# Optimization experiments

Measured on AMD Instinct MI355X. Metric: run time of the kernel, lower is better.

The kernel has to match this reference:

```python
import jax, jax.numpy as jnp
import numpy as np

TOP_K = 2
NUM_EXPERTS = 8
CAPACITY_FACTOR = 1.0


def setup_inputs() -> dict:
    key = jax.random.key(0)
    k1, k2, k3, k4 = jax.random.split(key, 4)
    sl, bs, hs, ffn = 2048, 2, 1024, 4096
    x = jax.random.normal(k1, (sl, bs, hs), dtype=jnp.float32)
    router_w = jax.random.normal(k2, (hs, NUM_EXPERTS), dtype=jnp.float32) * 0.02
    w1 = jax.random.normal(k3, (NUM_EXPERTS, hs, ffn), dtype=jnp.float32) * 0.02
    w2 = jax.random.normal(k4, (NUM_EXPERTS, ffn, hs), dtype=jnp.float32) * 0.02
    bias = jnp.zeros((1, 1, hs), dtype=jnp.float32)
    return {"x": x, "router_w": router_w, "w1": w1, "w2": w2, "bias": bias}


def _moe_forward(x, router_w, w1, w2):
    sl, bs, hs = x.shape
    xf = x.reshape(-1, hs)                                   # [T, H]
    T = xf.shape[0]
    TK = T * TOP_K
    capacity = int(CAPACITY_FACTOR * TOP_K * T / NUM_EXPERTS)  # static

    # Router: softmax over experts, then top-k (LearnedRouter)
    scores = jax.nn.softmax(xf @ router_w, axis=-1)          # [T, E]
    expert_weights, top_experts = jax.lax.top_k(scores, TOP_K)  # [T, K]
    ew = expert_weights.reshape(-1)                          # [T*K]
    te = top_experts.reshape(-1).astype(jnp.int32)           # [T*K]

    # indices_and_bins: stable sort by expert id + histogram + inclusive cumsum
    indices = jnp.argsort(te, stable=True)                   # sorted pos -> flat slot
    tokens_per_expert = jnp.zeros((NUM_EXPERTS,), jnp.int32).at[te].add(1)
    bins = jnp.cumsum(tokens_per_expert)                     # inclusive cumsum
    starts = bins - tokens_per_expert                        # exclusive offsets

    # binned_gather -> [E, capacity, H]; tokens beyond capacity are dropped
    c_range = jnp.arange(capacity)
    pos = starts[:, None] + c_range[None, :]                 # [E, C] positions in sorted order
    valid = c_range[None, :] < tokens_per_expert[:, None]    # [E, C]
    slot = indices[jnp.clip(pos, 0, TK - 1)]                 # flat (token*K + k) slot
    tok = slot // TOP_K                                      # source token row
    gathered = jnp.where(valid[..., None], xf[tok], 0.0)     # [E, C, H]

    # grouped expert MLP: gelu(x @ w1) @ w2  (megablocks mlp.MLP)
    h = jax.nn.gelu(jnp.einsum('ech,ehf->ecf', gathered, w1))
    y = jnp.einsum('ecf,efh->ech', h, w2)                    # [E, C, H]

    # binned_scatter: weighted accumulate back to token rows
    p = jnp.arange(TK)
    e_of_p = jnp.searchsorted(bins, p, side='right')         # expert of sorted pos
    c_of_p = p - starts[e_of_p]                              # slot within expert bin
    ok = c_of_p < capacity                                   # dropped tokens contribute 0
    vals = jnp.where(ok[:, None], y[e_of_p, jnp.clip(c_of_p, 0, capacity - 1)], 0.0)
    flat = indices                                           # flat slot at sorted pos p
    w = ew[flat]
    out = jnp.zeros((T, hs), x.dtype).at[flat // TOP_K].add(w[:, None] * vals)
    return out.reshape(sl, bs, hs)


def reference(x, router_w, w1, w2, bias):
    out = _moe_forward(x, router_w, w1, w2)
    return (out, bias)
```

## Files before the change

kernel.cpp:

```cpp
#include <hip/hip_runtime.h>
#include <hip/hip_bf16.h>


#define T_TOK 4096
#define HS 1024
#define FFN 4096
#define NE 8
#define CAP 1024
#define TKS 8192

#define WS_TE   67108864
#define WS_EW   67141632
#define WS_PERM 67174400
#define WS_WT   67239936
#define WS_XB   134348800

typedef float f4 __attribute__((ext_vector_type(4)));
typedef __bf16 bf16x8 __attribute__((ext_vector_type(8)));
typedef float f32x4 __attribute__((ext_vector_type(4)));

__device__ __forceinline__ void gld_lds16(const void* g, void* l) {
    __builtin_amdgcn_global_load_lds(
        (const __attribute__((address_space(1))) unsigned int*)g,
        (__attribute__((address_space(3))) unsigned int*)l, 16, 0, 0);
}

__global__ void init_out_kernel(float* __restrict__ out, const float* __restrict__ bias) {
    int i = blockIdx.x * 256 + threadIdx.x;
    const int TH = T_TOK * HS;
    if (i < TH) out[i] = 0.0f;
    else if (i < TH + HS) out[i] = bias[i - TH];
}

__global__ __launch_bounds__(256) void router_kernel(const float* __restrict__ x,
                                                     const float* __restrict__ rw,
                                                     int* __restrict__ te,
                                                     float* __restrict__ ew,
                                                     __bf16* __restrict__ xb) {
    __shared__ float rwt[NE * HS];
    int tid = threadIdx.x;
    for (int i = tid; i < NE * HS; i += 256) {
        int h = i >> 3, e = i & 7;
        rwt[e * HS + h] = rw[i];
    }
    __syncthreads();
    int wave = tid >> 6, lane = tid & 63;
    int t = blockIdx.x * 4 + wave;
    const float* xr = x + (size_t)t * HS;
    float s[NE];
    float xv[16];
#pragma unroll
    for (int e = 0; e < NE; ++e) s[e] = 0.0f;
#pragma unroll
    for (int j = 0; j < 16; ++j) {
        int h = lane + j * 64;
        xv[j] = xr[h];
#pragma unroll
        for (int e = 0; e < NE; ++e) s[e] += xv[j] * rwt[e * HS + h];
    }
#pragma unroll
    for (int j = 0; j < 16; ++j)
        xb[(size_t)t * HS + lane + j * 64] = (__bf16)xv[j];
#pragma unroll
    for (int e = 0; e < NE; ++e) {
#pragma unroll
        for (int off = 1; off < 64; off <<= 1) s[e] += __shfl_xor(s[e], off, 64);
    }
    float m = s[0];
#pragma unroll
    for (int e = 1; e < NE; ++e) m = fmaxf(m, s[e]);
    float psum = 0.0f;
#pragma unroll
    for (int e = 0; e < NE; ++e) psum += __expf(s[e] - m);
    int e0 = 0; float v0 = s[0];
#pragma unroll
    for (int e = 1; e < NE; ++e) { if (s[e] > v0) { v0 = s[e]; e0 = e; } }
    int e1 = -1; float v1 = -1e30f;
#pragma unroll
    for (int e = 0; e < NE; ++e) { if (e != e0 && s[e] > v1) { v1 = s[e]; e1 = e; } }
    if (lane == 0) {
        float inv = 1.0f / psum;
        te[2 * t]     = e0;
        te[2 * t + 1] = e1;
        ew[2 * t]     = __expf(v0 - m) * inv;
        ew[2 * t + 1] = __expf(v1 - m) * inv;
    }
}

__global__ __launch_bounds__(256) void sort_kernel(const int* __restrict__ te,
                                                   int* __restrict__ perm) {
    __shared__ int hist[256 * NE];
    int tid = threadIdx.x;
#pragma unroll
    for (int e = 0; e < NE; ++e) hist[tid * NE + e] = 0;
    for (int i = tid; i < TKS; i += 256) perm[i] = -1;
    __syncthreads();
    for (int j = 0; j < 32; ++j) {
        int p = tid * 32 + j;
        hist[tid * NE + te[p]]++;
    }
    __syncthreads();
    if (tid < NE) {
        int run = 0;
        for (int i = 0; i < 256; ++i) {
            int v = hist[i * NE + tid];
            hist[i * NE + tid] = run;
            run += v;
        }
    }
    __syncthreads();
    for (int j = 0; j < 32; ++j) {
        int p = tid * 32 + j;
        int e = te[p];
        int c = hist[tid * NE + e]++;
        if (c < CAP) perm[e * CAP + c] = p;
    }
}

__global__ __launch_bounds__(256) void conv_wt_kernel(const float* __restrict__ w,
                                                      __bf16* __restrict__ wt,
                                                      int K, int N) {
    __shared__ __bf16 t[64][72];
    const int e = blockIdx.z;
    const int kb = blockIdx.y * 64, nb = blockIdx.x * 64;
    const int tid = threadIdx.x;
    const float* src = w + ((size_t)e * K + kb) * N + nb;
    {
        const int kk = tid >> 4, nc = (tid & 15) * 4;
#pragma unroll
        for (int i = 0; i < 4; ++i) {
            int k = kk + 16 * i;
            f4 v = *(const f4*)(src + (size_t)k * N + nc);
            t[nc + 0][k] = (__bf16)v[0];
            t[nc + 1][k] = (__bf16)v[1];
            t[nc + 2][k] = (__bf16)v[2];
            t[nc + 3][k] = (__bf16)v[3];
        }
    }
    __syncthreads();
    __bf16* dst = wt + ((size_t)e * N + nb) * K + kb;
    const int nn = tid >> 3, ch = (tid & 7) * 8;
#pragma unroll
    for (int i = 0; i < 2; ++i) {
        int n = nn + 32 * i;
        bf16x8 v = *(const bf16x8*)(&t[n][ch]);
        *(bf16x8*)(dst + (size_t)n * K + ch) = v;
    }
}


#define PBAR() do {                                                         \
    asm volatile("" ::: "memory");                                          \
    __builtin_amdgcn_s_barrier();                                           \
    asm volatile("" ::: "memory");                                          \
} while (0)

#define WAITV(N_) asm volatile("s_waitcnt vmcnt(" #N_ ")" ::: "memory")

#define STAGE_A(cb_, h_, koff_) do {                                        \
    gld_lds16(aptr[(h_)*2 + 0] + (koff_), &As[cb_][(h_)*128 + w*16 + 0][0]);\
    gld_lds16(aptr[(h_)*2 + 1] + (koff_), &As[cb_][(h_)*128 + w*16 + 8][0]);\
} while (0)

#define STAGE_B(cb_, h_, koff_) do {                                        \
    gld_lds16(bptr[(h_)*2 + 0] + (koff_), &Bs[cb_][(h_)*128 + w*16 + 0][0]);\
    gld_lds16(bptr[(h_)*2 + 1] + (koff_), &Bs[cb_][(h_)*128 + w*16 + 8][0]);\
} while (0)

#define STAGE_TILE(cb_, koff_) do {                                         \
    STAGE_A(cb_, 0, koff_); STAGE_A(cb_, 1, koff_);                         \
    STAGE_B(cb_, 0, koff_); STAGE_B(cb_, 1, koff_);                         \
} while (0)

#define RD_A4(MB_) do {                                                     \
    _Pragma("unroll")                                                       \
    for (int mi = 0; mi < 4; ++mi)                                          \
        _Pragma("unroll")                                                   \
        for (int kk = 0; kk < 2; ++kk)                                      \
            a[mi][kk] = *(const bf16x8*)&As[c][wr*128 + ((MB_)+mi)*16 + l15]\
                            [((kk*4 + (lane>>4)) ^ (lane&7)) * 8];          \
} while (0)

#define RD_B2(NB_) do {                                                     \
    _Pragma("unroll")                                                       \
    for (int ni = 0; ni < 2; ++ni)                                          \
        _Pragma("unroll")                                                   \
        for (int kk = 0; kk < 2; ++kk)                                      \
            b[(NB_)+ni][kk] = *(const bf16x8*)&Bs[c][wc*64 + ((NB_)+ni)*16 + l15]\
                            [((kk*4 + (lane>>4)) ^ (lane&7)) * 8];          \
} while (0)

#define MFMA16(MB_, NB_) do {                                               \
    __builtin_amdgcn_s_setprio(1);                                          \
    _Pragma("unroll")                                                       \
    for (int mi = 0; mi < 4; ++mi)                                          \
        _Pragma("unroll")                                                   \
        for (int ni = 0; ni < 2; ++ni)                                      \
            _Pragma("unroll")                                               \
            for (int kk = 0; kk < 2; ++kk)                                  \
                acc[(MB_)+mi][(NB_)+ni] = __builtin_amdgcn_mfma_f32_16x16x32_bf16(\
                    a[mi][kk], b[(NB_)+ni][kk], acc[(MB_)+mi][(NB_)+ni], 0, 0, 0);\
    __builtin_amdgcn_s_setprio(0);                                          \
} while (0)

#define KLOOP(NT_)                                                          \
    STAGE_TILE(0, 0);                                                       \
    STAGE_TILE(1, 64);                                                      \
    for (int t = 0; t < (NT_); ++t) {                                       \
        const int c = t & 1;                                                \
        if (t == (NT_) - 1) WAITV(0); else WAITV(8);                        \
        PBAR();                                                             \
                                                               \
        RD_A4(0); RD_B2(0);                                                 \
        PBAR();                                                             \
        MFMA16(0, 0);                                                       \
        PBAR();                                                             \
                                                               \
        RD_B2(2);                                                           \
        PBAR();                                                             \
        MFMA16(0, 2);                                                       \
        PBAR();                                                             \
                                                               \
        RD_A4(4);                                                           \
        PBAR();                                                             \
        MFMA16(4, 2);                                                       \
        PBAR();                                                             \
               \
        if (t + 2 < (NT_)) STAGE_TILE(c, (t + 2) * 64);                     \
        __builtin_amdgcn_sched_barrier(0);                                  \
        MFMA16(4, 0);                                                       \
    }

__global__ __launch_bounds__(512, 2) void gemm1_kernel(const __bf16* __restrict__ xb,
                                                       const __bf16* __restrict__ w1t,
                                                       const int* __restrict__ perm,
                                                       __bf16* __restrict__ hbuf) {
    __shared__ __bf16 As[2][256][64];
    __shared__ __bf16 Bs[2][256][64];
    const int hw = blockIdx.x + 16 * blockIdx.y + 64 * blockIdx.z;
    const int logical = (hw & 7) * 64 + (hw >> 3);
    const int nblk = logical & 15;
    const int mblk = (logical >> 4) & 3;
    const int e    = logical >> 6;
    const int tid = threadIdx.x, lane = tid & 63, w = tid >> 6;
    const int wr = w >> 2, wc = w & 3;
    const int l15 = lane & 15;
    const int srl = lane >> 3;
    const int gsrc = (lane & 7) ^ srl;

    const __bf16* aptr[4];
    const __bf16* bptr[4];
#pragma unroll
    for (int h = 0; h < 2; ++h) {
#pragma unroll
        for (int o = 0; o < 2; ++o) {
            int r = h * 128 + w * 16 + o * 8 + srl;
            int p = perm[e * CAP + mblk * 256 + r];
            int tok = (p < 0) ? 0 : (p >> 1);
            aptr[h * 2 + o] = xb + (size_t)tok * HS + gsrc * 8;
            int brow = nblk * 256 + r;
            bptr[h * 2 + o] = w1t + ((size_t)e * FFN + brow) * HS + gsrc * 8;
        }
    }

    f32x4 acc[8][4];
#pragma unroll
    for (int mi = 0; mi < 8; ++mi)
#pragma unroll
        for (int ni = 0; ni < 4; ++ni) acc[mi][ni] = (f32x4)0.0f;
    bf16x8 a[4][2], b[4][2];

    KLOOP(HS / 64)

    const int mbase = mblk * 256 + wr * 128;
    const int nbase = nblk * 256 + wc * 64;
#pragma unroll
    for (int mi = 0; mi < 8; ++mi) {
#pragma unroll
        for (int ni = 0; ni < 4; ++ni) {
#pragma unroll
            for (int reg = 0; reg < 4; ++reg) {
                int mrow = mbase + mi * 16 + (lane >> 4) * 4 + reg;
                int ncol = nbase + ni * 16 + l15;
                float z = acc[mi][ni][reg];
                float z2 = z * z;
                float y = z * (1.5957691216057308f + 0.07135481627f * z2);
                float ex = __expf(-y);
                float gv = z * __builtin_amdgcn_rcpf(1.0f + ex);
                hbuf[(size_t)(e * CAP + mrow) * FFN + ncol] = (__bf16)gv;
            }
        }
    }
}

__global__ __launch_bounds__(512, 2) void gemm2_kernel(const __bf16* __restrict__ hbuf,
                                                       const __bf16* __restrict__ w2t,
                                                       const int* __restrict__ perm,
                                                       const float* __restrict__ ew,
                                                       float* __restrict__ out) {
    __shared__ __bf16 As[2][256][64];
    __shared__ __bf16 Bs[2][256][64];
    const int hw = blockIdx.x + 4 * blockIdx.y + 16 * blockIdx.z;
    const int logical = (hw & 7) * 32 + (hw >> 3);
    const int nblk = logical & 3;
    const int mblk = (logical >> 2) & 3;
    const int zz   = logical >> 4;
    const int e    = zz >> 1, half = zz & 1;
    const int tid = threadIdx.x, lane = tid & 63, w = tid >> 6;
    const int wr = w >> 2, wc = w & 3;
    const int l15 = lane & 15;
    const int srl = lane >> 3;
    const int gsrc = (lane & 7) ^ srl;
    const size_t kbase = (size_t)half * 2048;

    const __bf16* aptr[4];
    const __bf16* bptr[4];
#pragma unroll
    for (int h = 0; h < 2; ++h) {
#pragma unroll
        for (int o = 0; o < 2; ++o) {
            int r = h * 128 + w * 16 + o * 8 + srl;
            aptr[h * 2 + o] = hbuf + ((size_t)(e * CAP + mblk * 256 + r)) * FFN
                              + kbase + gsrc * 8;
            int brow = nblk * 256 + r;
            bptr[h * 2 + o] = w2t + ((size_t)e * HS + brow) * FFN
                              + kbase + gsrc * 8;
        }
    }

    f32x4 acc[8][4];
#pragma unroll
    for (int mi = 0; mi < 8; ++mi)
#pragma unroll
        for (int ni = 0; ni < 4; ++ni) acc[mi][ni] = (f32x4)0.0f;
    bf16x8 a[4][2], b[4][2];

    KLOOP(2048 / 64)

    __syncthreads();
    int* sperm = (int*)&As[0][0][0];
    float* swt = (float*)(sperm + 256);
    if (tid < 256) {
        int p = perm[e * CAP + mblk * 256 + tid];
        sperm[tid] = p;
        swt[tid] = (p >= 0) ? ew[p] : 0.0f;
    }
    __syncthreads();

    const int nbase = nblk * 256 + wc * 64;
#pragma unroll
    for (int mi = 0; mi < 8; ++mi) {
#pragma unroll
        for (int reg = 0; reg < 4; ++reg) {
            int mloc = wr * 128 + mi * 16 + (lane >> 4) * 4 + reg;
            int p = sperm[mloc];
            if (p >= 0) {
                int tok = p >> 1;
                float wgt = swt[mloc];
#pragma unroll
                for (int ni = 0; ni < 4; ++ni) {
                    int n = nbase + ni * 16 + l15;
                    atomicAdd(&out[(size_t)tok * HS + n], wgt * acc[mi][ni][reg]);
                }
            }
        }
    }
}

extern "C" void kernel_launch(void* const* d_in, const int* in_sizes, int n_in,
                              void* d_out, int out_size, void* d_ws, size_t ws_size,
                              hipStream_t stream) {
    const float* x    = (const float*)d_in[0];
    const float* rw   = (const float*)d_in[1];
    const float* w1   = (const float*)d_in[2];
    const float* w2   = (const float*)d_in[3];
    const float* bias = (const float*)d_in[4];
    float* out = (float*)d_out;
    char* ws = (char*)d_ws;

    __bf16* hbuf = (__bf16*)ws;
    int*    te   = (int*)(ws + WS_TE);
    float*  ew   = (float*)(ws + WS_EW);
    int*    perm = (int*)(ws + WS_PERM);
    __bf16* wt   = (__bf16*)(ws + WS_WT);
    __bf16* xb   = (__bf16*)(ws + WS_XB);

    hipLaunchKernelGGL(init_out_kernel, dim3((T_TOK * HS + HS + 255) / 256), dim3(256),
                       0, stream, out, bias);
    hipLaunchKernelGGL(router_kernel, dim3(T_TOK / 4), dim3(256), 0, stream,
                       x, rw, te, ew, xb);
    hipLaunchKernelGGL(sort_kernel, dim3(1), dim3(256), 0, stream, te, perm);
    hipLaunchKernelGGL(conv_wt_kernel, dim3(FFN / 64, HS / 64, NE), dim3(256),
                       0, stream, w1, wt, HS, FFN);
    hipLaunchKernelGGL(gemm1_kernel, dim3(FFN / 256, CAP / 256, NE), dim3(512),
                       0, stream, xb, wt, perm, hbuf);
    hipLaunchKernelGGL(conv_wt_kernel, dim3(HS / 64, FFN / 64, NE), dim3(256),
                       0, stream, w2, wt, FFN, HS);
    hipLaunchKernelGGL(gemm2_kernel, dim3(HS / 256, CAP / 256, NE * 2), dim3(512),
                       0, stream, hbuf, wt, perm, ew, out);
}
```

Measured before the change: 290.3 us.

## Interleave async tile staging across MFMA phases with explicit LDS reads

The GEMM K-loop's global-to-LDS staging is split into pieces and spread across the four MFMA phases instead of issuing a whole tile at the end of each iteration. As soon as the current buffer's A rows are consumed, part of the next stage is issued into them early. LDS reads now go through inline-asm ds_read_b128 with explicit lgkmcnt(0) waits and schedule barriers, so the compiler cannot reorder them. This aims to smooth memory issue and overlap loads with matrix math, but adds barriers and fixed waits, and the early writes into live buffers carry hazard risk.

```diff
diff --git a/kernel.cpp b/kernel.cpp
--- a/kernel.cpp
+++ b/kernel.cpp
@@ -23,6 +23,13 @@
     __builtin_amdgcn_global_load_lds(
         (const __attribute__((address_space(1))) unsigned int*)g,
         (__attribute__((address_space(3))) unsigned int*)l, 16, 0, 0);
+}
+
+__device__ __forceinline__ bf16x8 ds_read16(const void* p) {
+    bf16x8 r;
+    unsigned off = (unsigned)(size_t)(const __attribute__((address_space(3))) char*)p;
+    asm volatile("ds_read_b128 %0, %1" : "=&v"(r) : "v"(off));
+    return r;
 }
 
 __global__ void init_out_kernel(float* __restrict__ out, const float* __restrict__ bias) {
@@ -157,6 +164,11 @@
 
 #define WAITV(N_) asm volatile("s_waitcnt vmcnt(" #N_ ")" ::: "memory")
 
+#define LGKM0() do {                                                        \
+    asm volatile("s_waitcnt lgkmcnt(0)" ::: "memory");                      \
+    __builtin_amdgcn_sched_barrier(0);                                      \
+} while (0)
+
 #define STAGE_A(cb_, h_, koff_) do {                                        \
     gld_lds16(aptr[(h_)*2 + 0] + (koff_), &As[cb_][(h_)*128 + w*16 + 0][0]);\
     gld_lds16(aptr[(h_)*2 + 1] + (koff_), &As[cb_][(h_)*128 + w*16 + 8][0]);\
@@ -165,11 +177,6 @@
 #define STAGE_B(cb_, h_, koff_) do {                                        \
     gld_lds16(bptr[(h_)*2 + 0] + (koff_), &Bs[cb_][(h_)*128 + w*16 + 0][0]);\
     gld_lds16(bptr[(h_)*2 + 1] + (koff_), &Bs[cb_][(h_)*128 + w*16 + 8][0]);\
-} while (0)
-
-#define STAGE_TILE(cb_, koff_) do {                                         \
-    STAGE_A(cb_, 0, koff_); STAGE_A(cb_, 1, koff_);                         \
-    STAGE_B(cb_, 0, koff_); STAGE_B(cb_, 1, koff_);                         \
 } while (0)
 
 #define RD_A4(MB_) do {                                                     \
@@ -177,8 +184,8 @@
     for (int mi = 0; mi < 4; ++mi)                                          \
         _Pragma("unroll")                                                   \
         for (int kk = 0; kk < 2; ++kk)                                      \
-            a[mi][kk] = *(const bf16x8*)&As[c][wr*128 + ((MB_)+mi)*16 + l15]\
-                            [((kk*4 + (lane>>4)) ^ (lane&7)) * 8];          \
+            a[mi][kk] = ds_read16(&As[c][wr*128 + ((MB_)+mi)*16 + l15]      \
+                            [(((kk*4 + (lane>>4)) ^ (lane&7)) * 8)]);       \
 } while (0)
 
 #define RD_B2(NB_) do {                                                     \
@@ -186,8 +193,8 @@
     for (int ni = 0; ni < 2; ++ni)                                          \
         _Pragma("unroll")                                                   \
         for (int kk = 0; kk < 2; ++kk)                                      \
-            b[(NB_)+ni][kk] = *(const bf16x8*)&Bs[c][wc*64 + ((NB_)+ni)*16 + l15]\
-                            [((kk*4 + (lane>>4)) ^ (lane&7)) * 8];          \
+            b[(NB_)+ni][kk] = ds_read16(&Bs[c][wc*64 + ((NB_)+ni)*16 + l15] \
+                            [(((kk*4 + (lane>>4)) ^ (lane&7)) * 8)]);       \
 } while (0)
 
 #define MFMA16(MB_, NB_) do {                                               \
@@ -204,31 +211,37 @@
 } while (0)
 
 #define KLOOP(NT_)                                                          \
-    STAGE_TILE(0, 0);                                                       \
-    STAGE_TILE(1, 64);                                                      \
+    STAGE_B(0, 0, 0); STAGE_B(0, 1, 0);                                     \
+    STAGE_A(0, 0, 0); STAGE_A(0, 1, 0);                                     \
+    STAGE_B(1, 0, 64); STAGE_B(1, 1, 64);                                   \
+    STAGE_A(1, 0, 64);                                                      \
     for (int t = 0; t < (NT_); ++t) {                                       \
-        const int c = t & 1;                                                \
-        if (t == (NT_) - 1) WAITV(0); else WAITV(8);                        \
-        PBAR();                                                             \
-                                                               \
+        const int c = t & 1, o = c ^ 1;                                     \
+        if (t == (NT_) - 1) WAITV(0); else WAITV(6);                        \
+        PBAR();                                                             \
+                   \
         RD_A4(0); RD_B2(0);                                                 \
-        PBAR();                                                             \
+        if (t + 1 < (NT_)) STAGE_A(o, 1, (t + 1) * 64);                     \
+        PBAR(); LGKM0();                                                    \
         MFMA16(0, 0);                                                       \
         PBAR();                                                             \
-                                                               \
+                                                  \
         RD_B2(2);                                                           \
-        PBAR();                                                             \
+        PBAR(); LGKM0();                                                    \
         MFMA16(0, 2);                                                       \
         PBAR();                                                             \
-                                                               \
+               \
         RD_A4(4);                                                           \
-        PBAR();                                                             \
+        if (t + 2 < (NT_)) STAGE_B(c, 0, (t + 2) * 64);                     \
+        PBAR(); LGKM0();                                                    \
         MFMA16(4, 2);                                                       \
         PBAR();                                                             \
-               \
-        if (t + 2 < (NT_)) STAGE_TILE(c, (t + 2) * 64);                     \
-        __builtin_amdgcn_sched_barrier(0);                                  \
+                     \
+        if (t + 2 < (NT_)) { STAGE_B(c, 1, (t + 2) * 64);                   \
+                             STAGE_A(c, 0, (t + 2) * 64); }                 \
+        PBAR();                                                             \
         MFMA16(4, 0);                                                       \
+        PBAR();                                                             \
     }
 
 __global__ __launch_bounds__(512, 2) void gemm1_kernel(const __bf16* __restrict__ xb,
@@ -253,13 +266,13 @@
 #pragma unroll
     for (int h = 0; h < 2; ++h) {
 #pragma unroll
-        for (int o = 0; o < 2; ++o) {
-            int r = h * 128 + w * 16 + o * 8 + srl;
+        for (int o2 = 0; o2 < 2; ++o2) {
+            int r = h * 128 + w * 16 + o2 * 8 + srl;
             int p = perm[e * CAP + mblk * 256 + r];
             int tok = (p < 0) ? 0 : (p >> 1);
-            aptr[h * 2 + o] = xb + (size_t)tok * HS + gsrc * 8;
+            aptr[h * 2 + o2] = xb + (size_t)tok * HS + gsrc * 8;
             int brow = nblk * 256 + r;
-            bptr[h * 2 + o] = w1t + ((size_t)e * FFN + brow) * HS + gsrc * 8;
+            bptr[h * 2 + o2] = w1t + ((size_t)e * FFN + brow) * HS + gsrc * 8;
         }
     }
 
@@ -318,13 +331,13 @@
 #pragma unroll
     for (int h = 0; h < 2; ++h) {
 #pragma unroll
-        for (int o = 0; o < 2; ++o) {
-            int r = h * 128 + w * 16 + o * 8 + srl;
-            aptr[h * 2 + o] = hbuf + ((size_t)(e * CAP + mblk * 256 + r)) * FFN
-                              + kbase + gsrc * 8;
+        for (int o2 = 0; o2 < 2; ++o2) {
+            int r = h * 128 + w * 16 + o2 * 8 + srl;
+            aptr[h * 2 + o2] = hbuf + ((size_t)(e * CAP + mblk * 256 + r)) * FFN
+                               + kbase + gsrc * 8;
             int brow = nblk * 256 + r;
-            bptr[h * 2 + o] = w2t + ((size_t)e * HS + brow) * FFN
-                              + kbase + gsrc * 8;
+            bptr[h * 2 + o2] = w2t + ((size_t)e * HS + brow) * FFN
+                               + kbase + gsrc * 8;
         }
     }
 
```

After: 276.6 us (median of 2 runs). -4.7%, faster.
